# Performance work log

Measured on AMD Instinct MI355X. Metric: run time of the kernel, lower is better.

The kernel has to match this reference:

```python
import jax, jax.numpy as jnp
import numpy as np

B, L, D, V = 512, 128, 512, 100000

def setup_inputs() -> dict:
    key = jax.random.key(0)
    ks = jax.random.split(key, 8)
    return {
        "t1s": jax.random.randint(ks[0], (B,), 0, V),
        "t2s": jax.random.randint(ks[1], (B,), 0, V),
        "t1_contexts": jax.random.randint(ks[2], (B, L), 0, V),
        "t2_contexts": jax.random.randint(ks[3], (B, L), 0, V),
        "embed_table": jax.random.normal(ks[4], (V, D), dtype=jnp.float32),
        "att_mat": jax.random.normal(ks[5], (D, D), dtype=jnp.float32) * (6.0 / (D + D)) ** 0.5,
        "w_pred": jax.random.normal(ks[6], (D, 1), dtype=jnp.float32) * 0.02,
        "b_pred": jnp.zeros((1,), dtype=jnp.float32),
    }

def _frob_normalize(x):
    # torch.norm(mat, p=2) is the Frobenius norm of the whole (L, D) matrix
    n = jnp.sqrt(jnp.sum(x * x, axis=(1, 2), keepdims=True))
    return x / n

def reference(t1s, t2s, t1_contexts, t2_contexts, embed_table, att_mat, w_pred, b_pred):
    # dropout is identity in eval mode; t1s/t2s embeddings are unused in the
    # 'dynamic' branch (dead code in the original forward).
    A = _frob_normalize(embed_table[t1_contexts])  # (B, L, D)
    Bm = _frob_normalize(embed_table[t2_contexts])  # (B, L, D)
    # batched bilinear attention: tanh(A @ att_mat @ B^T)
    S = jnp.tanh(jnp.einsum('bld,de,bme->blm', A, att_mat, Bm))  # (B, L, L)
    rows = jax.nn.softmax(jnp.mean(S, axis=2), axis=1)  # (B, L)
    cols = jax.nn.softmax(jnp.mean(S, axis=1), axis=1)  # (B, L)
    newA = jnp.einsum('bld,bl->bd', A, rows)   # (B, D)
    newB = jnp.einsum('bld,bl->bd', Bm, cols)  # (B, D)
    logits = ((newA * newB) @ w_pred + b_pred).reshape(-1)  # (B,)
    return logits, S
```

## Files before the change

kernel.cpp:

```cpp
#include <hip/hip_runtime.h>
#include <hip/hip_bf16.h>
#include <stdint.h>

#define NB 512
#define NL 128
#define ND 512

typedef __bf16 bf16;
typedef __bf16 bf16x8 __attribute__((ext_vector_type(8)));
typedef float  f32x4  __attribute__((ext_vector_type(4)));

#define GLDS(src, dst) __builtin_amdgcn_global_load_lds( \
    (const __attribute__((address_space(1))) void*)(src), \
    (__attribute__((address_space(3))) void*)(dst), 16, 0, 0)

__global__ __launch_bounds__(256) void k_attT(const float* __restrict__ att,
                                              bf16* __restrict__ attT) {
    int i = blockIdx.x * 256 + threadIdx.x;
    int n = i >> 9, k = i & 511;
    attT[i] = (bf16)att[k * 512 + n];
}

__global__ __launch_bounds__(512, 4) void k_mega(
        const int* __restrict__ ctx1, const int* __restrict__ ctx2,
        const float* __restrict__ table, const bf16* __restrict__ attT,
        bf16* __restrict__ Ab, bf16* __restrict__ Bb,
        float* __restrict__ Sout, const float* __restrict__ w_pred,
        const float* __restrict__ b_pred, float* __restrict__ logits) {
    const int b = blockIdx.x, row0 = b * NL, tid = threadIdx.x;
    const int lane = tid & 63, w = tid >> 6;
    const int lm = lane & 15, quad = lane >> 4;
    const int wm = (w & 1) * 64;
    const int wn = (w >> 1) * 32;

    __shared__ __align__(16) char smem[69888];
    bf16* st0 = (bf16*)smem;
    bf16* st1 = (bf16*)(smem + 16384);
    bf16* Tch = (bf16*)(smem + 32768);
    float* pA   = (float*)smem;
    float* pB   = (float*)(smem + 16384);
    float* red  = (float*)(smem + 65536);
    float* red2 = (float*)(smem + 65600);
    float* rowb = (float*)(smem + 65664);
    float* colb = (float*)(smem + 67712);
    float* wrow = (float*)(smem + 68736);
    float* wcol = (float*)(smem + 69248);

    const int r8 = tid >> 6, c8 = tid & 63;
    float pa = 0.f, pb = 0.f;
    #pragma unroll 4
    for (int j = 0; j < 16; ++j) {
        int l = j * 8 + r8;
        int ia = ctx1[row0 + l], ib = ctx2[row0 + l];
        const float4* ra = (const float4*)table + (size_t)ia * (ND / 4) + c8 * 2;
        const float4* rb = (const float4*)table + (size_t)ib * (ND / 4) + c8 * 2;
        float4 a0 = ra[0], a1 = ra[1];
        float4 b0 = rb[0], b1 = rb[1];
        pa += a0.x*a0.x + a0.y*a0.y + a0.z*a0.z + a0.w*a0.w
            + a1.x*a1.x + a1.y*a1.y + a1.z*a1.z + a1.w*a1.w;
        pb += b0.x*b0.x + b0.y*b0.y + b0.z*b0.z + b0.w*b0.w
            + b1.x*b1.x + b1.y*b1.y + b1.z*b1.z + b1.w*b1.w;
        union { bf16 h[8]; uint4 u; } ua, ub;
        ua.h[0]=(bf16)a0.x; ua.h[1]=(bf16)a0.y; ua.h[2]=(bf16)a0.z; ua.h[3]=(bf16)a0.w;
        ua.h[4]=(bf16)a1.x; ua.h[5]=(bf16)a1.y; ua.h[6]=(bf16)a1.z; ua.h[7]=(bf16)a1.w;
        ub.h[0]=(bf16)b0.x; ub.h[1]=(bf16)b0.y; ub.h[2]=(bf16)b0.z; ub.h[3]=(bf16)b0.w;
        ub.h[4]=(bf16)b1.x; ub.h[5]=(bf16)b1.y; ub.h[6]=(bf16)b1.z; ub.h[7]=(bf16)b1.w;
        *(uint4*)(Ab + (size_t)(row0 + l) * ND + c8 * 8) = ua.u;
        *(uint4*)(Bb + (size_t)(row0 + l) * ND + c8 * 8) = ub.u;
    }
    for (int o = 32; o; o >>= 1) { pa += __shfl_xor(pa, o); pb += __shfl_xor(pb, o); }
    if (lane == 0) { red[w * 2] = pa; red[w * 2 + 1] = pb; }
    __syncthreads();
    float ssA = 0.f, ssB = 0.f;
    #pragma unroll
    for (int i = 0; i < 8; ++i) { ssA += red[i * 2]; ssB += red[i * 2 + 1]; }

    f32x4 accS[4][2] = {};

    for (int nc = 0; nc < 4; ++nc) {
        const bf16* attN = attT + (size_t)(nc * 128) * ND;
        f32x4 acc1[4][2] = {};

        for (int t8 = 0; t8 < 8; ++t8) {
            const int k0 = t8 * 64;
            #pragma unroll
            for (int i = 0; i < 2; ++i) {
                int s = i * 512 + tid, r = s >> 3, c = (s & 7) ^ (r & 7);
                GLDS(Ab + (size_t)(row0 + r) * ND + k0 + c * 8, st0 + s * 8);
                GLDS(attN + (size_t)r * ND + k0 + c * 8, st1 + s * 8);
            }
            __syncthreads();
            #pragma unroll
            for (int kk = 0; kk < 2; ++kk) {
                bf16x8 af[4], bf2[2];
                const int ca = (kk * 4 + quad) ^ (lm & 7);
                #pragma unroll
                for (int t4 = 0; t4 < 4; ++t4)
                    af[t4] = *(const bf16x8*)&st0[(wm + t4 * 16 + lm) * 64 + ca * 8];
                #pragma unroll
                for (int t2 = 0; t2 < 2; ++t2)
                    bf2[t2] = *(const bf16x8*)&st1[(wn + t2 * 16 + lm) * 64 + ca * 8];
                #pragma unroll
                for (int im = 0; im < 4; ++im)
                    #pragma unroll
                    for (int jn = 0; jn < 2; ++jn)
                        acc1[im][jn] = __builtin_amdgcn_mfma_f32_16x16x32_bf16(
                            af[im], bf2[jn], acc1[im][jn], 0, 0, 0);
            }
            __syncthreads();
        }

        #pragma unroll
        for (int i = 0; i < 2; ++i) {
            int s = i * 512 + tid, r = s >> 3, c = (s & 7) ^ (r & 7);
            GLDS(Bb + (size_t)(row0 + r) * ND + nc * 128 + c * 8, st0 + s * 8);
            GLDS(Bb + (size_t)(row0 + r) * ND + nc * 128 + 64 + c * 8, st1 + s * 8);
        }
        #pragma unroll
        for (int im = 0; im < 4; ++im)
        #pragma unroll
        for (int jn = 0; jn < 2; ++jn)
        #pragma unroll
        for (int p = 0; p < 4; ++p) {
            int m = wm + im * 16 + quad * 4 + p;
            int n = wn + jn * 16 + lm;
            int ks = n >> 6, c = n & 63;
            int pos = (((c >> 3) ^ (m & 7)) << 3) + (c & 7);
            Tch[ks * 8192 + m * 64 + pos] = (bf16)acc1[im][jn][p];
        }
        __syncthreads();

        #pragma unroll
        for (int th = 0; th < 2; ++th) {
            const bf16* Bs_ = th ? st1 : st0;
            const bf16* Tk  = Tch + th * 8192;
            #pragma unroll
            for (int kk = 0; kk < 2; ++kk) {
                bf16x8 af[4], bf2[2];
                const int ca = (kk * 4 + quad) ^ (lm & 7);
                #pragma unroll
                for (int t4 = 0; t4 < 4; ++t4)
                    af[t4] = *(const bf16x8*)&Tk[(wm + t4 * 16 + lm) * 64 + ca * 8];
                #pragma unroll
                for (int t2 = 0; t2 < 2; ++t2)
                    bf2[t2] = *(const bf16x8*)&Bs_[(wn + t2 * 16 + lm) * 64 + ca * 8];
                #pragma unroll
                for (int im = 0; im < 4; ++im)
                    #pragma unroll
                    for (int jn = 0; jn < 2; ++jn)
                        accS[im][jn] = __builtin_amdgcn_mfma_f32_16x16x32_bf16(
                            af[im], bf2[jn], accS[im][jn], 0, 0, 0);
            }
        }
        __syncthreads();
    }

    const float sc = rsqrtf(ssA * ssB);
    float* __restrict__ Sb = Sout + (size_t)b * NL * NL;
    #pragma unroll
    for (int im = 0; im < 4; ++im)
    #pragma unroll
    for (int jn = 0; jn < 2; ++jn)
    #pragma unroll
    for (int p = 0; p < 4; ++p) {
        float v = tanhf(accS[im][jn][p] * sc);
        accS[im][jn][p] = v;
        int m = wm + im * 16 + quad * 4 + p;
        int n = wn + jn * 16 + lm;
        __builtin_nontemporal_store(v, &Sb[m * NL + n]);
    }
    #pragma unroll
    for (int im = 0; im < 4; ++im)
    #pragma unroll
    for (int p = 0; p < 4; ++p) {
        float r = accS[im][0][p] + accS[im][1][p];
        r += __shfl_xor(r, 1); r += __shfl_xor(r, 2);
        r += __shfl_xor(r, 4); r += __shfl_xor(r, 8);
        if (lm == 0) rowb[(w >> 1) * NL + wm + im * 16 + quad * 4 + p] = r;
    }
    #pragma unroll
    for (int jn = 0; jn < 2; ++jn) {
        float cv = 0.f;
        #pragma unroll
        for (int im = 0; im < 4; ++im)
            #pragma unroll
            for (int p = 0; p < 4; ++p) cv += accS[im][jn][p];
        cv += __shfl_xor(cv, 16); cv += __shfl_xor(cv, 32);
        if (quad == 0) colb[(w & 1) * NL + wn + jn * 16 + lm] = cv;
    }
    __syncthreads();

    if (tid < 64) {
        float a  = (rowb[tid] + rowb[NL + tid] + rowb[2 * NL + tid] + rowb[3 * NL + tid]) * (1.f / NL);
        float c2 = (rowb[tid + 64] + rowb[NL + tid + 64] + rowb[2 * NL + tid + 64] + rowb[3 * NL + tid + 64]) * (1.f / NL);
        float mx = fmaxf(a, c2);
        for (int o = 32; o; o >>= 1) mx = fmaxf(mx, __shfl_xor(mx, o));
        float e0 = expf(a - mx), e1 = expf(c2 - mx);
        float s = e0 + e1;
        for (int o = 32; o; o >>= 1) s += __shfl_xor(s, o);
        float inv = 1.f / s;
        wrow[tid] = e0 * inv; wrow[tid + 64] = e1 * inv;
    } else if (tid < 128) {
        int q = tid - 64;
        float a  = (colb[q] + colb[NL + q]) * (1.f / NL);
        float c2 = (colb[q + 64] + colb[NL + q + 64]) * (1.f / NL);
        float mx = fmaxf(a, c2);
        for (int o = 32; o; o >>= 1) mx = fmaxf(mx, __shfl_xor(mx, o));
        float e0 = expf(a - mx), e1 = expf(c2 - mx);
        float s = e0 + e1;
        for (int o = 32; o; o >>= 1) s += __shfl_xor(s, o);
        float inv = 1.f / s;
        wcol[q] = e0 * inv; wcol[q + 64] = e1 * inv;
    }
    __syncthreads();

    const int c = tid & 63, g = tid >> 6;
    const bf16* __restrict__ Abase = Ab + (size_t)b * NL * ND;
    const bf16* __restrict__ Bbase = Bb + (size_t)b * NL * ND;
    float aacc[8] = {}, bacc[8] = {};
    for (int l = g; l < NL; l += 8) {
        float wr = wrow[l], wc = wcol[l];
        bf16x8 va = *(const bf16x8*)(Abase + (size_t)l * ND + c * 8);
        bf16x8 vb = *(const bf16x8*)(Bbase + (size_t)l * ND + c * 8);
        #pragma unroll
        for (int j = 0; j < 8; ++j) {
            aacc[j] += wr * (float)va[j];
            bacc[j] += wc * (float)vb[j];
        }
    }
    #pragma unroll
    for (int j = 0; j < 8; ++j) {
        pA[g * ND + c * 8 + j] = aacc[j];
        pB[g * ND + c * 8 + j] = bacc[j];
    }
    __syncthreads();

    if (tid < 64) {
        float dot = 0.f;
        #pragma unroll
        for (int j = 0; j < 8; ++j) {
            int d = tid * 8 + j;
            float na = 0.f, nb = 0.f;
            #pragma unroll
            for (int g2 = 0; g2 < 8; ++g2) {
                na += pA[g2 * ND + d];
                nb += pB[g2 * ND + d];
            }
            dot += na * nb * w_pred[d];
        }
        for (int o = 32; o; o >>= 1) dot += __shfl_xor(dot, o);
        if (tid == 0)
            logits[b] = dot * rsqrtf(ssA) * rsqrtf(ssB) + b_pred[0];
    }
}

extern "C" void kernel_launch(void* const* d_in, const int* in_sizes, int n_in,
                              void* d_out, int out_size, void* d_ws, size_t ws_size,
                              hipStream_t stream) {
    const int*   t1c = (const int*)d_in[2];
    const int*   t2c = (const int*)d_in[3];
    const float* emb = (const float*)d_in[4];
    const float* att = (const float*)d_in[5];
    const float* wp  = (const float*)d_in[6];
    const float* bp  = (const float*)d_in[7];

    float* out    = (float*)d_out;
    float* logits = out;
    float* S      = out + NB;

    char* ws = (char*)d_ws;
    bf16*  Ab   = (bf16*)(ws);
    bf16*  Bb   = (bf16*)(ws + 67108864);
    bf16*  attT = (bf16*)(ws + 134217728);

    k_attT<<<dim3(1024), 256, 0, stream>>>(att, attT);
    k_mega<<<dim3(NB), 512, 0, stream>>>(t1c, t2c, emb, attT, Ab, Bb,
                                         S, wp, bp, logits);
}
```

Baseline: 453.9 us.

## Split embedding gather into separate kernel and double-buffer first GEMM loads

Moves the embedding gather, bf16 conversion and per-batch sum-of-squares into a separate widely-parallel kernel, with per-batch norms accumulated by atomics. The attention-matrix transpose is folded into the same launch. The main kernel's first GEMM now uses 32-wide K tiles with double-buffered async global-to-LDS loads and explicit waitcnt, plus s_setprio around the MFMA blocks. The goal is more memory-level parallelism for the random gather and overlap of loads with MFMA, at the cost of an extra memset and launch and an Ab/Bb round trip through memory between kernels.

```diff
diff --git a/kernel.cpp b/kernel.cpp
--- a/kernel.cpp
+++ b/kernel.cpp
@@ -14,18 +14,54 @@
     (const __attribute__((address_space(1))) void*)(src), \
     (__attribute__((address_space(3))) void*)(dst), 16, 0, 0)
 
-__global__ __launch_bounds__(256) void k_attT(const float* __restrict__ att,
-                                              bf16* __restrict__ attT) {
-    int i = blockIdx.x * 256 + threadIdx.x;
-    int n = i >> 9, k = i & 511;
-    attT[i] = (bf16)att[k * 512 + n];
+__global__ __launch_bounds__(256) void k_gather(const int* __restrict__ ctx1,
+                                                const int* __restrict__ ctx2,
+                                                const float* __restrict__ table,
+                                                bf16* __restrict__ d1,
+                                                bf16* __restrict__ d2,
+                                                float* __restrict__ ss,
+                                                const float* __restrict__ att,
+                                                bf16* __restrict__ attT) {
+    const int b = blockIdx.x, side = blockIdx.y, zc = blockIdx.z, t = threadIdx.x;
+    if (side == 2) {
+        int chunk = b * 8 + zc;
+        if (chunk < 1024) {
+            int i = chunk * 256 + t;
+            int n = i >> 9, k = i & 511;
+            attT[i] = (bf16)att[k * 512 + n];
+        }
+        return;
+    }
+    const int* __restrict__ ctx = side ? ctx2 : ctx1;
+    bf16* __restrict__ dst = side ? d2 : d1;
+    const int base = b * NL;
+    const int dv = t & 127, lr = t >> 7;
+    int idxs[8];
+    #pragma unroll
+    for (int i = 0; i < 8; ++i) idxs[i] = ctx[base + zc * 16 + i * 2 + lr];
+    float acc = 0.f;
+    #pragma unroll
+    for (int i = 0; i < 8; ++i) {
+        int l = zc * 16 + i * 2 + lr;
+        f32x4 v = __builtin_nontemporal_load(
+            (const f32x4*)table + (size_t)idxs[i] * (ND / 4) + dv);
+        acc += v[0]*v[0] + v[1]*v[1] + v[2]*v[2] + v[3]*v[3];
+        union { bf16 h[4]; uint2 u; } pk;
+        pk.h[0] = (bf16)v[0]; pk.h[1] = (bf16)v[1];
+        pk.h[2] = (bf16)v[2]; pk.h[3] = (bf16)v[3];
+        *((uint2*)(dst + (size_t)(base + l) * ND) + dv) = pk.u;
+    }
+    for (int o = 32; o; o >>= 1) acc += __shfl_xor(acc, o);
+    __shared__ float red[4];
+    if ((t & 63) == 0) red[t >> 6] = acc;
+    __syncthreads();
+    if (t == 0) atomicAdd(&ss[side * NB + b], red[0] + red[1] + red[2] + red[3]);
 }
 
-__global__ __launch_bounds__(512, 4) void k_mega(
-        const int* __restrict__ ctx1, const int* __restrict__ ctx2,
-        const float* __restrict__ table, const bf16* __restrict__ attT,
-        bf16* __restrict__ Ab, bf16* __restrict__ Bb,
-        float* __restrict__ Sout, const float* __restrict__ w_pred,
+__global__ __launch_bounds__(512, 4) void k_mega3(
+        const bf16* __restrict__ Ab, const bf16* __restrict__ attT,
+        const bf16* __restrict__ Bb, float* __restrict__ Sout,
+        const float* __restrict__ ss, const float* __restrict__ w_pred,
         const float* __restrict__ b_pred, float* __restrict__ logits) {
     const int b = blockIdx.x, row0 = b * NL, tid = threadIdx.x;
     const int lane = tid & 63, w = tid >> 6;
@@ -34,46 +70,17 @@
     const int wn = (w >> 1) * 32;
 
     __shared__ __align__(16) char smem[69888];
-    bf16* st0 = (bf16*)smem;
-    bf16* st1 = (bf16*)(smem + 16384);
     bf16* Tch = (bf16*)(smem + 32768);
     float* pA   = (float*)smem;
     float* pB   = (float*)(smem + 16384);
-    float* red  = (float*)(smem + 65536);
     float* red2 = (float*)(smem + 65600);
     float* rowb = (float*)(smem + 65664);
     float* colb = (float*)(smem + 67712);
     float* wrow = (float*)(smem + 68736);
     float* wcol = (float*)(smem + 69248);
 
-    const int r8 = tid >> 6, c8 = tid & 63;
-    float pa = 0.f, pb = 0.f;
-    #pragma unroll 4
-    for (int j = 0; j < 16; ++j) {
-        int l = j * 8 + r8;
-        int ia = ctx1[row0 + l], ib = ctx2[row0 + l];
-        const float4* ra = (const float4*)table + (size_t)ia * (ND / 4) + c8 * 2;
-        const float4* rb = (const float4*)table + (size_t)ib * (ND / 4) + c8 * 2;
-        float4 a0 = ra[0], a1 = ra[1];
-        float4 b0 = rb[0], b1 = rb[1];
-        pa += a0.x*a0.x + a0.y*a0.y + a0.z*a0.z + a0.w*a0.w
-            + a1.x*a1.x + a1.y*a1.y + a1.z*a1.z + a1.w*a1.w;
-        pb += b0.x*b0.x + b0.y*b0.y + b0.z*b0.z + b0.w*b0.w
-            + b1.x*b1.x + b1.y*b1.y + b1.z*b1.z + b1.w*b1.w;
-        union { bf16 h[8]; uint4 u; } ua, ub;
-        ua.h[0]=(bf16)a0.x; ua.h[1]=(bf16)a0.y; ua.h[2]=(bf16)a0.z; ua.h[3]=(bf16)a0.w;
-        ua.h[4]=(bf16)a1.x; ua.h[5]=(bf16)a1.y; ua.h[6]=(bf16)a1.z; ua.h[7]=(bf16)a1.w;
-        ub.h[0]=(bf16)b0.x; ub.h[1]=(bf16)b0.y; ub.h[2]=(bf16)b0.z; ub.h[3]=(bf16)b0.w;
-        ub.h[4]=(bf16)b1.x; ub.h[5]=(bf16)b1.y; ub.h[6]=(bf16)b1.z; ub.h[7]=(bf16)b1.w;
-        *(uint4*)(Ab + (size_t)(row0 + l) * ND + c8 * 8) = ua.u;
-        *(uint4*)(Bb + (size_t)(row0 + l) * ND + c8 * 8) = ub.u;
-    }
-    for (int o = 32; o; o >>= 1) { pa += __shfl_xor(pa, o); pb += __shfl_xor(pb, o); }
-    if (lane == 0) { red[w * 2] = pa; red[w * 2 + 1] = pb; }
-    __syncthreads();
-    float ssA = 0.f, ssB = 0.f;
-    #pragma unroll
-    for (int i = 0; i < 8; ++i) { ssA += red[i * 2]; ssB += red[i * 2 + 1]; }
+    const int rT = tid >> 2, slT = tid & 3;
+    const int csT = slT ^ ((rT >> 1) & 3);
 
     f32x4 accS[4][2] = {};
 
@@ -81,41 +88,49 @@
         const bf16* attN = attT + (size_t)(nc * 128) * ND;
         f32x4 acc1[4][2] = {};
 
-        for (int t8 = 0; t8 < 8; ++t8) {
-            const int k0 = t8 * 64;
-            #pragma unroll
-            for (int i = 0; i < 2; ++i) {
-                int s = i * 512 + tid, r = s >> 3, c = (s & 7) ^ (r & 7);
-                GLDS(Ab + (size_t)(row0 + r) * ND + k0 + c * 8, st0 + s * 8);
-                GLDS(attN + (size_t)r * ND + k0 + c * 8, st1 + s * 8);
-            }
-            __syncthreads();
-            #pragma unroll
-            for (int kk = 0; kk < 2; ++kk) {
-                bf16x8 af[4], bf2[2];
-                const int ca = (kk * 4 + quad) ^ (lm & 7);
+        GLDS(Ab + (size_t)(row0 + rT) * ND + csT * 8, (bf16*)smem + tid * 8);
+        GLDS(attN + (size_t)rT * ND + csT * 8, (bf16*)(smem + 8192) + tid * 8);
+
+        for (int t = 0; t < 16; ++t) {
+            if (t < 15) {
+                const int k0 = (t + 1) * 32, p = (t + 1) & 1;
+                GLDS(Ab + (size_t)(row0 + rT) * ND + k0 + csT * 8,
+                     (bf16*)(smem + p * 16384) + tid * 8);
+                GLDS(attN + (size_t)rT * ND + k0 + csT * 8,
+                     (bf16*)(smem + p * 16384 + 8192) + tid * 8);
+                asm volatile("s_waitcnt vmcnt(2)" ::: "memory");
+            } else {
+                asm volatile("s_waitcnt vmcnt(0)" ::: "memory");
+            }
+            __builtin_amdgcn_s_barrier();
+            const bf16* A_ = (bf16*)(smem + (t & 1) * 16384);
+            const bf16* N_ = (bf16*)(smem + (t & 1) * 16384 + 8192);
+            bf16x8 af[4], bf2[2];
+            #pragma unroll
+            for (int t4 = 0; t4 < 4; ++t4) {
+                int R = wm + t4 * 16 + lm;
+                af[t4] = *(const bf16x8*)&A_[R * 32 + (quad ^ ((R >> 1) & 3)) * 8];
+            }
+            #pragma unroll
+            for (int t2 = 0; t2 < 2; ++t2) {
+                int R = wn + t2 * 16 + lm;
+                bf2[t2] = *(const bf16x8*)&N_[R * 32 + (quad ^ ((R >> 1) & 3)) * 8];
+            }
+            __builtin_amdgcn_s_setprio(1);
+            #pragma unroll
+            for (int im = 0; im < 4; ++im)
                 #pragma unroll
-                for (int t4 = 0; t4 < 4; ++t4)
-                    af[t4] = *(const bf16x8*)&st0[(wm + t4 * 16 + lm) * 64 + ca * 8];
-                #pragma unroll
-                for (int t2 = 0; t2 < 2; ++t2)
-                    bf2[t2] = *(const bf16x8*)&st1[(wn + t2 * 16 + lm) * 64 + ca * 8];
-                #pragma unroll
-                for (int im = 0; im < 4; ++im)
-                    #pragma unroll
-                    for (int jn = 0; jn < 2; ++jn)
-                        acc1[im][jn] = __builtin_amdgcn_mfma_f32_16x16x32_bf16(
-                            af[im], bf2[jn], acc1[im][jn], 0, 0, 0);
-            }
-            __syncthreads();
-        }
-
-        #pragma unroll
-        for (int i = 0; i < 2; ++i) {
-            int s = i * 512 + tid, r = s >> 3, c = (s & 7) ^ (r & 7);
-            GLDS(Bb + (size_t)(row0 + r) * ND + nc * 128 + c * 8, st0 + s * 8);
-            GLDS(Bb + (size_t)(row0 + r) * ND + nc * 128 + 64 + c * 8, st1 + s * 8);
-        }
+                for (int jn = 0; jn < 2; ++jn)
+                    acc1[im][jn] = __builtin_amdgcn_mfma_f32_16x16x32_bf16(
+                        af[im], bf2[jn], acc1[im][jn], 0, 0, 0);
+            __builtin_amdgcn_s_setprio(0);
+            __builtin_amdgcn_s_barrier();
+        }
+
+        #pragma unroll
+        for (int i = 0; i < 4; ++i)
+            GLDS(Bb + (size_t)(row0 + rT) * ND + nc * 128 + i * 32 + csT * 8,
+                 (bf16*)(smem + i * 8192) + tid * 8);
         #pragma unroll
         for (int im = 0; im < 4; ++im)
         #pragma unroll
@@ -130,20 +145,23 @@
         }
         __syncthreads();
 
+        __builtin_amdgcn_s_setprio(1);
         #pragma unroll
         for (int th = 0; th < 2; ++th) {
-            const bf16* Bs_ = th ? st1 : st0;
-            const bf16* Tk  = Tch + th * 8192;
+            const bf16* Tk = Tch + th * 8192;
             #pragma unroll
             for (int kk = 0; kk < 2; ++kk) {
+                const bf16* Bs_ = (bf16*)(smem + (th * 2 + kk) * 8192);
+                const int ca = (kk * 4 + quad) ^ (lm & 7);
                 bf16x8 af[4], bf2[2];
-                const int ca = (kk * 4 + quad) ^ (lm & 7);
                 #pragma unroll
                 for (int t4 = 0; t4 < 4; ++t4)
                     af[t4] = *(const bf16x8*)&Tk[(wm + t4 * 16 + lm) * 64 + ca * 8];
                 #pragma unroll
-                for (int t2 = 0; t2 < 2; ++t2)
-                    bf2[t2] = *(const bf16x8*)&Bs_[(wn + t2 * 16 + lm) * 64 + ca * 8];
+                for (int t2 = 0; t2 < 2; ++t2) {
+                    int R = wn + t2 * 16 + lm;
+                    bf2[t2] = *(const bf16x8*)&Bs_[R * 32 + (quad ^ ((R >> 1) & 3)) * 8];
+                }
                 #pragma unroll
                 for (int im = 0; im < 4; ++im)
                     #pragma unroll
@@ -152,9 +170,11 @@
                             af[im], bf2[jn], accS[im][jn], 0, 0, 0);
             }
         }
+        __builtin_amdgcn_s_setprio(0);
         __syncthreads();
     }
 
+    const float ssA = ss[b], ssB = ss[NB + b];
     const float sc = rsqrtf(ssA * ssB);
     float* __restrict__ Sb = Sout + (size_t)b * NL * NL;
     #pragma unroll
@@ -272,8 +292,9 @@
     bf16*  Ab   = (bf16*)(ws);
     bf16*  Bb   = (bf16*)(ws + 67108864);
     bf16*  attT = (bf16*)(ws + 134217728);
-
-    k_attT<<<dim3(1024), 256, 0, stream>>>(att, attT);
-    k_mega<<<dim3(NB), 512, 0, stream>>>(t1c, t2c, emb, attT, Ab, Bb,
-                                         S, wp, bp, logits);
+    float* ss   = (float*)(ws + 134742016);
+
+    hipMemsetAsync(ss, 0, 4096, stream);
+    k_gather<<<dim3(NB, 3, 8), 256, 0, stream>>>(t1c, t2c, emb, Ab, Bb, ss, att, attT);
+    k_mega3<<<dim3(NB), 512, 0, stream>>>(Ab, attT, Bb, S, ss, wp, bp, logits);
 }
```

Result: no change. 446.3 us (-1.7%).
